# Kernel tuning notes

Hardware: AMD Instinct MI355X
Metric: run time of the kernel (lower is better)

Reference implementation:

```python
import jax, jax.numpy as jnp
import numpy as np

B, H, I = 16384, 512, 256
EPS = 1e-8

def setup_inputs() -> dict:
    key = jax.random.key(0)
    ks = jax.random.split(key, 10)
    x = jax.random.normal(ks[0], (B, I), dtype=jnp.float32)
    hx_re = jax.random.normal(ks[1], (B, H), dtype=jnp.float32) * 0.05
    hx_im = jax.random.normal(ks[2], (B, H), dtype=jnp.float32) * 0.05
    # diag = exp(1j * U(-pi, pi)) -> store angles as real params
    diag_angles = jax.random.uniform(ks[3], (3 * H,), dtype=jnp.float32,
                                     minval=-np.pi, maxval=np.pi)
    # rotation = U(0,1)*2 - (1+1j): real part in [-1,1], imag part in [-1,1]
    rot_re = jax.random.uniform(ks[4], (2 * H,), dtype=jnp.float32) * 2.0 - 1.0
    rot_im = jax.random.uniform(ks[5], (2 * H,), dtype=jnp.float32) * 2.0 - 1.0
    # xavier-scale complex Linear weight (hidden, input), no bias
    w_scale = float(np.sqrt(2.0 / (I + H)))
    W_re = jax.random.normal(ks[6], (H, I), dtype=jnp.float32) * w_scale
    W_im = jax.random.normal(ks[7], (H, I), dtype=jnp.float32) * w_scale
    beta = jnp.zeros((H,), dtype=jnp.float32)  # ModReLU bias, zeros init
    perm = jax.random.permutation(ks[8], H).astype(jnp.int32)
    return {"x": x, "hx_re": hx_re, "hx_im": hx_im,
            "diag_angles": diag_angles, "rot_re": rot_re, "rot_im": rot_im,
            "W_re": W_re, "W_im": W_im, "beta": beta, "perm": perm}

def _unit(v):
    # complex_unit_norm: v / (||v|| + eps), norm over last dim
    return v / (jnp.linalg.norm(v) + EPS)

def _apply_householder(h, v):
    # h @ (I - 2 v v^H) == h - 2 (h @ v) v^H  (rank-1 form, no NxN matrix)
    return h - 2.0 * (h @ v)[:, None] * jnp.conj(v)[None, :]

def reference(x, hx_re, hx_im, diag_angles, rot_re, rot_im, W_re, W_im, beta, perm):
    diag = jnp.exp(1j * diag_angles)                 # complex64, |.| = 1
    d1, d2, d3 = jnp.split(diag, 3)
    rot = rot_re + 1j * rot_im
    r1, r2 = jnp.split(rot, 2)
    v1 = _unit(r1)
    v2 = _unit(r2)

    h = hx_re + 1j * hx_im                           # (B, H) complex64
    h = jnp.fft.fft(d1[None, :] * h, axis=-1)        # D1 then F
    h = _apply_householder(h, v1)                    # R1
    h = jnp.fft.ifft(d2[None, :] * h[:, perm], axis=-1)  # Pi, D2, F^-1
    h = d3[None, :] * _apply_householder(h, v2)      # R2 then D3
    # complex Linear on real input: x @ W^T with complex W
    emb = (x @ W_re.T) + 1j * (x @ W_im.T)
    h = h + emb
    # ModReLU: relu(|z| + beta) * exp(1j * angle(z))
    mag = jnp.abs(h)
    out = jax.nn.relu(mag + beta[None, :]) * jnp.exp(1j * jnp.angle(h))
    # return as real (B, H, 2) [real, imag] for real-valued harness
    return jnp.stack([out.real, out.imag], axis=-1)
```

## Files before the change

### kernel.cpp

```cpp
#include <hip/hip_runtime.h>
#include <hip/hip_bf16.h>
#include <stdint.h>
#include <stddef.h>

typedef __bf16 bf16;
typedef bf16 bf16x8 __attribute__((ext_vector_type(8)));
typedef float f32x4 __attribute__((ext_vector_type(4)));

#define EPSN 1e-8f
#define TWO_PI 6.283185307179586f

#define NB 16384
#define NH 512
#define NI 256
#define KTOT 1280

__device__ __forceinline__ float2 cmul(float2 a, float2 b) {
  return make_float2(a.x * b.x - a.y * b.y, a.x * b.y + a.y * b.x);
}
__device__ __forceinline__ float2 cmulconj(float2 a, float2 b) {
  return make_float2(a.x * b.x + a.y * b.y, a.y * b.x - a.x * b.y);
}
__device__ __forceinline__ float2 cadd(float2 a, float2 b) {
  return make_float2(a.x + b.x, a.y + b.y);
}
__device__ __forceinline__ int brev9(int i) {
  return (int)(__brev((unsigned)i) >> 23);
}

__device__ __forceinline__ void gload16(const bf16* g, bf16* l) {
  __builtin_amdgcn_global_load_lds(
      (const __attribute__((address_space(1))) void*)g,
      (__attribute__((address_space(3))) void*)l, 16, 0, 0);
}

__global__ __launch_bounds__(256) void build_U(
    const float* __restrict__ ang, const float* __restrict__ rre,
    const float* __restrict__ rim, const float* __restrict__ wre,
    const float* __restrict__ wim, const int* __restrict__ perm,
    bf16* __restrict__ Bm) {
  __shared__ float2 bufA[512];
  __shared__ float2 bufB[512];
  __shared__ float2 redw[4];
  __shared__ float2 bc;
  __shared__ float2 red2[256];

  const int t = threadIdx.x;
  const int j = blockIdx.x;
  const int j0 = t, j1 = t + 256;

  const float r1x0 = rre[j0], r1y0 = rim[j0];
  const float r1x1 = rre[j1], r1y1 = rim[j1];
  const float r2x0 = rre[512 + j0], r2y0 = rim[512 + j0];
  const float r2x1 = rre[512 + j1], r2y1 = rim[512 + j1];
  red2[t] = make_float2(r1x0 * r1x0 + r1y0 * r1y0 + r1x1 * r1x1 + r1y1 * r1y1,
                        r2x0 * r2x0 + r2y0 * r2y0 + r2x1 * r2x1 + r2y1 * r2y1);
  __syncthreads();
  for (int off = 128; off > 0; off >>= 1) {
    if (t < off) {
      red2[t].x += red2[t + off].x;
      red2[t].y += red2[t + off].y;
    }
    __syncthreads();
  }
  const float inv1 = 1.0f / (sqrtf(red2[0].x) + EPSN);
  const float inv2 = 1.0f / (sqrtf(red2[0].y) + EPSN);
  const float2 v1a = make_float2(r1x0 * inv1, r1y0 * inv1);
  const float2 v1b = make_float2(r1x1 * inv1, r1y1 * inv1);
  const float2 v2a = make_float2(r2x0 * inv2, r2y0 * inv2);
  const float2 v2b = make_float2(r2x1 * inv2, r2y1 * inv2);

  {
    float sj, cj;
    __sincosf(ang[j], &sj, &cj);
    const float2 dj = make_float2(cj, sj);
    float2 z = make_float2(0.f, 0.f);
    bufA[brev9(j0)] = (j0 == j) ? dj : z;
    bufA[brev9(j1)] = (j1 == j) ? dj : z;
  }
  __syncthreads();

#pragma unroll
  for (int st = 0; st < 9; ++st) {
    const int half = 1 << st;
    const int pos = t & (half - 1);
    const int i0 = ((t >> st) << (st + 1)) + pos;
    const int i1 = i0 + half;
    const float angv = -TWO_PI * (float)pos / (float)(2 << st);
    float sn, cs;
    __sincosf(angv, &sn, &cs);
    float2 u = bufA[i0];
    float2 w = bufA[i1];
    float2 tw = make_float2(cs * w.x - sn * w.y, cs * w.y + sn * w.x);
    bufA[i0] = make_float2(u.x + tw.x, u.y + tw.y);
    bufA[i1] = make_float2(u.x - tw.x, u.y - tw.y);
    __syncthreads();
  }

  {
    float2 p = cadd(cmul(bufA[j0], v1a), cmul(bufA[j1], v1b));
    for (int off = 32; off > 0; off >>= 1) {
      p.x += __shfl_down(p.x, off);
      p.y += __shfl_down(p.y, off);
    }
    if ((t & 63) == 0) redw[t >> 6] = p;
    __syncthreads();
    if (t == 0) bc = cadd(cadd(redw[0], redw[1]), cadd(redw[2], redw[3]));
    __syncthreads();
  }
  const float2 dot1 = bc;

  {
    float2 c0 = cmulconj(dot1, v1a);
    float2 c1 = cmulconj(dot1, v1b);
    float2 a0 = bufA[j0], a1 = bufA[j1];
    bufA[j0] = make_float2(a0.x - 2.f * c0.x, a0.y - 2.f * c0.y);
    bufA[j1] = make_float2(a1.x - 2.f * c1.x, a1.y - 2.f * c1.y);
  }
  __syncthreads();

  {
    int p0 = perm[j0], p1 = perm[j1];
    float s0, c0, s1, c1;
    __sincosf(ang[512 + j0], &s0, &c0);
    __sincosf(ang[512 + j1], &s1, &c1);
    float2 g0 = cmul(make_float2(c0, s0), bufA[p0]);
    float2 g1 = cmul(make_float2(c1, s1), bufA[p1]);
    bufB[brev9(j0)] = g0;
    bufB[brev9(j1)] = g1;
  }
  __syncthreads();

#pragma unroll
  for (int st = 0; st < 9; ++st) {
    const int half = 1 << st;
    const int pos = t & (half - 1);
    const int i0 = ((t >> st) << (st + 1)) + pos;
    const int i1 = i0 + half;
    const float angv = TWO_PI * (float)pos / (float)(2 << st);
    float sn, cs;
    __sincosf(angv, &sn, &cs);
    float2 u = bufB[i0];
    float2 w = bufB[i1];
    float2 tw = make_float2(cs * w.x - sn * w.y, cs * w.y + sn * w.x);
    bufB[i0] = make_float2(u.x + tw.x, u.y + tw.y);
    bufB[i1] = make_float2(u.x - tw.x, u.y - tw.y);
    __syncthreads();
  }

  {
    float2 q = cadd(cmul(bufB[j0], v2a), cmul(bufB[j1], v2b));
    for (int off = 32; off > 0; off >>= 1) {
      q.x += __shfl_down(q.x, off);
      q.y += __shfl_down(q.y, off);
    }
    if ((t & 63) == 0) redw[t >> 6] = q;
    __syncthreads();
    if (t == 0) bc = cadd(cadd(redw[0], redw[1]), cadd(redw[2], redw[3]));
    __syncthreads();
  }
  const float invN = 1.0f / 512.0f;
  const float2 dot2 = make_float2(bc.x * invN, bc.y * invN);

#pragma unroll
  for (int e = 0; e < 2; ++e) {
    const int i = (e == 0) ? j0 : j1;
    const float2 vj = (e == 0) ? v2a : v2b;
    float2 h2 = make_float2(bufB[i].x * invN, bufB[i].y * invN);
    float2 c2 = cmulconj(dot2, vj);
    float2 hh = make_float2(h2.x - 2.f * c2.x, h2.y - 2.f * c2.y);
    float s3, c3;
    __sincosf(ang[1024 + i], &s3, &c3);
    float2 u = cmul(make_float2(c3, s3), hh);
    bf16* r0 = Bm + (size_t)(2 * i) * KTOT;
    bf16* r1 = Bm + (size_t)(2 * i + 1) * KTOT;
    r0[j] = (bf16)u.x;
    r0[512 + j] = (bf16)(-u.y);
    r1[j] = (bf16)u.y;
    r1[512 + j] = (bf16)u.x;
  }

  Bm[(size_t)(2 * j) * KTOT + 1024 + t] = (bf16)wre[j * NI + t];
  Bm[(size_t)(2 * j + 1) * KTOT + 1024 + t] = (bf16)wim[j * NI + t];
}

__global__ __launch_bounds__(256) void pack_A(const float* __restrict__ hxre,
                                              const float* __restrict__ hxim,
                                              const float* __restrict__ x,
                                              bf16* __restrict__ Apack) {
  const int tid = blockIdx.x * 256 + threadIdx.x;
  const int b = tid / 160;
  const int o = tid - b * 160;
  const float* src;
  if (o < 64)
    src = hxre + (size_t)b * 512 + o * 8;
  else if (o < 128)
    src = hxim + (size_t)b * 512 + (o - 64) * 8;
  else
    src = x + (size_t)b * 256 + (o - 128) * 8;
  float4 f0 = ((const float4*)src)[0];
  float4 f1 = ((const float4*)src)[1];
  bf16x8 v;
  v[0] = (bf16)f0.x; v[1] = (bf16)f0.y; v[2] = (bf16)f0.z; v[3] = (bf16)f0.w;
  v[4] = (bf16)f1.x; v[5] = (bf16)f1.y; v[6] = (bf16)f1.z; v[7] = (bf16)f1.w;
  *(bf16x8*)(Apack + (size_t)b * KTOT + o * 8) = v;
}

__global__ __launch_bounds__(256) void gemm_fused(
    const bf16* __restrict__ Apack, const bf16* __restrict__ Bm,
    const float* __restrict__ beta, float* __restrict__ out) {
  __shared__ bf16 As[128 * 64];
  __shared__ bf16 Bs[128 * 64];

  const int t = threadIdx.x;
  const int lane = t & 63;
  const int wv = t >> 6;

  const int id = blockIdx.x;
  const int xcd = id & 7;
  const int lix = id >> 3;
  const int mBase = (xcd * 16 + (lix >> 3)) * 128;
  const int nBase = (lix & 7) * 128;

  const int srow = wv * 32 + (lane >> 3);
  const int soct = (lane & 7) ^ (lane >> 3);
  const bf16* gA = Apack + (size_t)(mBase + srow) * KTOT + soct * 8;
  const bf16* gB = Bm + (size_t)(nBase + srow) * KTOT + soct * 8;
  bf16* lA = As + (wv * 32) * 64;
  bf16* lB = Bs + (wv * 32) * 64;

  const int lr = lane & 15;
  const int lq = lane >> 4;
  const int waveM = wv & 1;
  const int waveN = wv >> 1;
  const int lrm = lr & 7;

  f32x4 acc[4][4] = {};

  for (int kk = 0; kk < KTOT; kk += 64) {
#pragma unroll
    for (int i = 0; i < 4; ++i) {
      gload16(gA + kk + (size_t)(i * 8) * KTOT, lA + i * 8 * 64);
      gload16(gB + kk + (size_t)(i * 8) * KTOT, lB + i * 8 * 64);
    }
    __syncthreads();

#pragma unroll
    for (int kh = 0; kh < 2; ++kh) {
      bf16x8 af[4], bfr[4];
#pragma unroll
      for (int mi = 0; mi < 4; ++mi)
        af[mi] = *(const bf16x8*)(&As[(waveM * 64 + mi * 16 + lr) * 64 +
                                      ((kh * 4 + lq) ^ lrm) * 8]);
#pragma unroll
      for (int ni = 0; ni < 4; ++ni)
        bfr[ni] = *(const bf16x8*)(&Bs[(waveN * 64 + ni * 16 + lr) * 64 +
                                       ((kh * 4 + lq) ^ lrm) * 8]);
#pragma unroll
      for (int mi = 0; mi < 4; ++mi)
#pragma unroll
        for (int ni = 0; ni < 4; ++ni)
          acc[mi][ni] = __builtin_amdgcn_mfma_f32_16x16x32_bf16(
              af[mi], bfr[ni], acc[mi][ni], 0, 0, 0);
    }
    __syncthreads();
  }

  const int col = lane & 15;
  const int row0 = (lane >> 4) * 4;
  const int parity = lane & 1;
#pragma unroll
  for (int ni = 0; ni < 4; ++ni) {
    const int n = nBase + waveN * 64 + ni * 16 + col;
    const float bet = beta[n >> 1];
#pragma unroll
    for (int mi = 0; mi < 4; ++mi) {
      const int mrow = mBase + waveM * 64 + mi * 16 + row0;
#pragma unroll
      for (int r = 0; r < 4; ++r) {
        float a = acc[mi][ni][r];
        float o = __shfl_xor(a, 1);
        float re = parity ? o : a;
        float im = parity ? a : o;
        float mag = sqrtf(re * re + im * im);
        float s = mag + bet;
        float val;
        if (s <= 0.f)
          val = 0.f;
        else if (mag > 0.f)
          val = (parity ? im : re) * (s / mag);
        else
          val = parity ? 0.f : s;
        out[(size_t)(mrow + r) * 1024 + n] = val;
      }
    }
  }
}

extern "C" void kernel_launch(void* const* d_in, const int* in_sizes, int n_in,
                              void* d_out, int out_size, void* d_ws,
                              size_t ws_size, hipStream_t stream) {
  const float* x = (const float*)d_in[0];
  const float* hxre = (const float*)d_in[1];
  const float* hxim = (const float*)d_in[2];
  const float* ang = (const float*)d_in[3];
  const float* rre = (const float*)d_in[4];
  const float* rim = (const float*)d_in[5];
  const float* wre = (const float*)d_in[6];
  const float* wim = (const float*)d_in[7];
  const float* beta = (const float*)d_in[8];
  const int* perm = (const int*)d_in[9];

  char* ws = (char*)d_ws;
  bf16* Bm = (bf16*)ws;
  bf16* Apack = (bf16*)(ws + (size_t)1024 * KTOT * 2);

  build_U<<<512, 256, 0, stream>>>(ang, rre, rim, wre, wim, perm, Bm);
  pack_A<<<(NB * 160) / 256, 256, 0, stream>>>(hxre, hxim, x, Apack);
  gemm_fused<<<1024, 256, 0, stream>>>(Apack, Bm, beta, (float*)d_out);
}
```

Measured before the change: 223.1 us.

## Merge prep kernels, use 8-wave GEMM blocks, and use rsqrt in ModReLU epilogue

The unitary-matrix build and the bf16 packing of the A operand now run as one launch, with extra blocks doing the packing. The GEMM block grows from 4 to 8 waves, each owning a 64x32 sub-tile instead of 64x64, so per-wave accumulators halve and more waves are available to hide latency. The epilogue replaces sqrt and divide with a single reciprocal square root. The cost is fewer MFMAs per LDS fragment load and tighter register limits from launch_bounds(512,4), which could cause spills.

```diff
diff --git a/kernel.cpp b/kernel.cpp
--- a/kernel.cpp
+++ b/kernel.cpp
@@ -34,19 +34,43 @@
       (__attribute__((address_space(3))) void*)l, 16, 0, 0);
 }
 
-__global__ __launch_bounds__(256) void build_U(
+__global__ __launch_bounds__(256) void prep(
     const float* __restrict__ ang, const float* __restrict__ rre,
     const float* __restrict__ rim, const float* __restrict__ wre,
     const float* __restrict__ wim, const int* __restrict__ perm,
-    bf16* __restrict__ Bm) {
+    const float* __restrict__ hxre, const float* __restrict__ hxim,
+    const float* __restrict__ x, bf16* __restrict__ Bm,
+    bf16* __restrict__ Apack) {
   __shared__ float2 bufA[512];
   __shared__ float2 bufB[512];
   __shared__ float2 redw[4];
   __shared__ float2 bc;
   __shared__ float2 red2[256];
 
+  const int bid = blockIdx.x;
   const int t = threadIdx.x;
-  const int j = blockIdx.x;
+
+  if (bid >= 512) {
+    const int tid = (bid - 512) * 256 + t;
+    const int b = tid / 160;
+    const int o = tid - b * 160;
+    const float* src;
+    if (o < 64)
+      src = hxre + (size_t)b * 512 + o * 8;
+    else if (o < 128)
+      src = hxim + (size_t)b * 512 + (o - 64) * 8;
+    else
+      src = x + (size_t)b * 256 + (o - 128) * 8;
+    float4 f0 = ((const float4*)src)[0];
+    float4 f1 = ((const float4*)src)[1];
+    bf16x8 v;
+    v[0] = (bf16)f0.x; v[1] = (bf16)f0.y; v[2] = (bf16)f0.z; v[3] = (bf16)f0.w;
+    v[4] = (bf16)f1.x; v[5] = (bf16)f1.y; v[6] = (bf16)f1.z; v[7] = (bf16)f1.w;
+    *(bf16x8*)(Apack + (size_t)b * KTOT + o * 8) = v;
+    return;
+  }
+
+  const int j = bid;
   const int j0 = t, j1 = t + 256;
 
   const float r1x0 = rre[j0], r1y0 = rim[j0];
@@ -184,29 +208,7 @@
   Bm[(size_t)(2 * j + 1) * KTOT + 1024 + t] = (bf16)wim[j * NI + t];
 }
 
-__global__ __launch_bounds__(256) void pack_A(const float* __restrict__ hxre,
-                                              const float* __restrict__ hxim,
-                                              const float* __restrict__ x,
-                                              bf16* __restrict__ Apack) {
-  const int tid = blockIdx.x * 256 + threadIdx.x;
-  const int b = tid / 160;
-  const int o = tid - b * 160;
-  const float* src;
-  if (o < 64)
-    src = hxre + (size_t)b * 512 + o * 8;
-  else if (o < 128)
-    src = hxim + (size_t)b * 512 + (o - 64) * 8;
-  else
-    src = x + (size_t)b * 256 + (o - 128) * 8;
-  float4 f0 = ((const float4*)src)[0];
-  float4 f1 = ((const float4*)src)[1];
-  bf16x8 v;
-  v[0] = (bf16)f0.x; v[1] = (bf16)f0.y; v[2] = (bf16)f0.z; v[3] = (bf16)f0.w;
-  v[4] = (bf16)f1.x; v[5] = (bf16)f1.y; v[6] = (bf16)f1.z; v[7] = (bf16)f1.w;
-  *(bf16x8*)(Apack + (size_t)b * KTOT + o * 8) = v;
-}
-
-__global__ __launch_bounds__(256) void gemm_fused(
+__global__ __launch_bounds__(512, 4) void gemm_fused(
     const bf16* __restrict__ Apack, const bf16* __restrict__ Bm,
     const float* __restrict__ beta, float* __restrict__ out) {
   __shared__ bf16 As[128 * 64];
@@ -222,44 +224,43 @@
   const int mBase = (xcd * 16 + (lix >> 3)) * 128;
   const int nBase = (lix & 7) * 128;
 
-  const int srow = wv * 32 + (lane >> 3);
-  const int soct = (lane & 7) ^ (lane >> 3);
+  const int subrow = lane >> 3;
+  const int soct = (lane & 7) ^ subrow;
+  const int srow = wv * 16 + subrow;
   const bf16* gA = Apack + (size_t)(mBase + srow) * KTOT + soct * 8;
   const bf16* gB = Bm + (size_t)(nBase + srow) * KTOT + soct * 8;
-  bf16* lA = As + (wv * 32) * 64;
-  bf16* lB = Bs + (wv * 32) * 64;
+  bf16* lA = As + (wv * 16) * 64;
+  bf16* lB = Bs + (wv * 16) * 64;
 
   const int lr = lane & 15;
   const int lq = lane >> 4;
+  const int lrm = lr & 7;
   const int waveM = wv & 1;
   const int waveN = wv >> 1;
-  const int lrm = lr & 7;
-
-  f32x4 acc[4][4] = {};
+
+  f32x4 acc[4][2] = {};
 
   for (int kk = 0; kk < KTOT; kk += 64) {
-#pragma unroll
-    for (int i = 0; i < 4; ++i) {
-      gload16(gA + kk + (size_t)(i * 8) * KTOT, lA + i * 8 * 64);
-      gload16(gB + kk + (size_t)(i * 8) * KTOT, lB + i * 8 * 64);
-    }
+    gload16(gA + kk, lA);
+    gload16(gA + kk + (size_t)8 * KTOT, lA + 8 * 64);
+    gload16(gB + kk, lB);
+    gload16(gB + kk + (size_t)8 * KTOT, lB + 8 * 64);
     __syncthreads();
 
 #pragma unroll
     for (int kh = 0; kh < 2; ++kh) {
-      bf16x8 af[4], bfr[4];
+      const int co = ((kh * 4 + lq) ^ lrm) * 8;
+      bf16x8 af[4], bfr[2];
 #pragma unroll
       for (int mi = 0; mi < 4; ++mi)
-        af[mi] = *(const bf16x8*)(&As[(waveM * 64 + mi * 16 + lr) * 64 +
-                                      ((kh * 4 + lq) ^ lrm) * 8]);
-#pragma unroll
-      for (int ni = 0; ni < 4; ++ni)
-        bfr[ni] = *(const bf16x8*)(&Bs[(waveN * 64 + ni * 16 + lr) * 64 +
-                                       ((kh * 4 + lq) ^ lrm) * 8]);
+        af[mi] = *(const bf16x8*)(&As[(waveM * 64 + mi * 16 + lr) * 64 + co]);
+#pragma unroll
+      for (int ni = 0; ni < 2; ++ni)
+        bfr[ni] = *(const bf16x8*)(&Bs[(waveN * 32 + ni * 16 + lr) * 64 + co]);
 #pragma unroll
       for (int mi = 0; mi < 4; ++mi)
 #pragma unroll
-        for (int ni = 0; ni < 4; ++ni)
+        for (int ni = 0; ni < 2; ++ni)
           acc[mi][ni] = __builtin_amdgcn_mfma_f32_16x16x32_bf16(
               af[mi], bfr[ni], acc[mi][ni], 0, 0, 0);
     }
@@ -267,11 +268,11 @@
   }
 
   const int col = lane & 15;
-  const int row0 = (lane >> 4) * 4;
+  const int row0 = lq * 4;
   const int parity = lane & 1;
 #pragma unroll
-  for (int ni = 0; ni < 4; ++ni) {
-    const int n = nBase + waveN * 64 + ni * 16 + col;
+  for (int ni = 0; ni < 2; ++ni) {
+    const int n = nBase + waveN * 32 + ni * 16 + col;
     const float bet = beta[n >> 1];
 #pragma unroll
     for (int mi = 0; mi < 4; ++mi) {
@@ -282,15 +283,15 @@
         float o = __shfl_xor(a, 1);
         float re = parity ? o : a;
         float im = parity ? a : o;
-        float mag = sqrtf(re * re + im * im);
-        float s = mag + bet;
+        float mag2 = re * re + im * im;
         float val;
-        if (s <= 0.f)
-          val = 0.f;
-        else if (mag > 0.f)
-          val = (parity ? im : re) * (s / mag);
-        else
-          val = parity ? 0.f : s;
+        if (mag2 > 0.f) {
+          float rs = __frsqrt_rn(mag2);
+          float s = mag2 * rs + bet;
+          val = (s > 0.f) ? (parity ? im : re) * (s * rs) : 0.f;
+        } else {
+          val = (bet > 0.f && parity == 0) ? bet : 0.f;
+        }
         out[(size_t)(mrow + r) * 1024 + n] = val;
       }
     }
@@ -315,7 +316,8 @@
   bf16* Bm = (bf16*)ws;
   bf16* Apack = (bf16*)(ws + (size_t)1024 * KTOT * 2);
 
-  build_U<<<512, 256, 0, stream>>>(ang, rre, rim, wre, wim, perm, Bm);
-  pack_A<<<(NB * 160) / 256, 256, 0, stream>>>(hxre, hxim, x, Apack);
-  gemm_fused<<<1024, 256, 0, stream>>>(Apack, Bm, beta, (float*)d_out);
-}
+  prep<<<512 + (NB * 160) / 256, 256, 0, stream>>>(ang, rre, rim, wre, wim,
+                                                   perm, hxre, hxim, x, Bm,
+                                                   Apack);
+  gemm_fused<<<1024, 512, 0, stream>>>(Apack, Bm, beta, (float*)d_out);
+}
```

New measurement: 200.4 us. 10.2% less time.
